# Kernel optimization log

Hardware: AMD Instinct MI355X
Metric: run time of the kernel (lower is better)

Reference implementation:

```python
import jax, jax.numpy as jnp
import numpy as np
from jax import lax

E, L, S, F = 4, 8, 512, 32
SAMPLE_SIZE = 512
BATCH_LEN = 64
TRAIN_ENVS = [0, 1, 2]


def setup_inputs() -> dict:
    key = jax.random.key(0)
    k1, k2 = jax.random.split(key)
    data_len = jax.random.randint(k2, (E, L), S // 2, S + 1).astype(jnp.int32)
    matrix = jax.random.normal(k1, (E, L, S, F), dtype=jnp.float32)
    # zero-pad samples beyond each (env,label) length, as shape_to_matrix does
    mask = (jnp.arange(S)[None, None, :, None] < data_len[:, :, None, None])
    matrix = matrix * mask.astype(jnp.float32)
    params = jnp.eye(F, dtype=jnp.float32)
    return {"matrix": matrix, "params": params, "data_len": data_len}


def _pair_indices():
    train_idx, test_idx = [], []
    for i in range(E):
        for j in range(E):
            idx = i * E + j
            if i < j:
                test_idx.append(idx)
                if i in TRAIN_ENVS and j in TRAIN_ENVS:
                    train_idx.append(idx)
    return np.array(train_idx), np.array(test_idx)


def reference(matrix, params, data_len):
    # normalize by mean per-(env,label,feature) std (torch.std is unbiased -> ddof=1)
    std = jnp.std(matrix, axis=2, ddof=1).mean()
    m = matrix / std
    bw = 1.06 * (S ** (-1.0 / 5.0)) * jnp.std(m, axis=2, ddof=1).mean()
    lenf = data_len.astype(jnp.float32)                     # [E,L]
    proj = jnp.einsum('elsf,fg->elsg', m, params)           # [E,L,S,F]

    left = lax.stop_gradient(proj.min())
    right = lax.stop_gradient(proj.max())
    delta = (right - left) / SAMPLE_SIZE
    grid = jnp.linspace(left, right, SAMPLE_SIZE)           # [G]
    divisor = jnp.sqrt(2.0 * jnp.pi) * bw

    n_chunks = SAMPLE_SIZE // BATCH_LEN
    grid_chunks = grid.reshape(n_chunks, BATCH_LEN)
    inv2bw2 = 0.5 / (bw * bw)
    pad_count = (float(S) - lenf)[:, :, None, None]         # [E,L,1,1]
    lend = lenf[:, :, None, None]

    def step(carry, pts):
        # Gaussian KDE kernel: offset^(d^2) == exp(-0.5*d^2/bw^2)
        d2 = (proj[..., None] - pts) ** 2                   # [E,L,S,F,C]
        ksum = jnp.exp(-inv2bw2 * d2).sum(axis=2)           # [E,L,F,C]
        corr = pad_count * jnp.exp(-inv2bw2 * pts ** 2)     # zero-padding correction
        red = (ksum - corr) / lend                          # [E,L,F,C]
        diff = jnp.abs(red[:, None] - red[None, :]).sum(-1) # [E,E,L,F]
        return carry + diff, None

    store, _ = lax.scan(step, jnp.zeros((E, E, L, F), dtype=proj.dtype), grid_chunks)
    store_dis = (store / divisor).reshape(E * E, L, F)

    train_idx, test_idx = _pair_indices()
    test_results = (store_dis[test_idx] * delta / 2.0).max(axis=0)    # [L,F]
    train_results = (store_dis[train_idx] * delta / 2.0).max(axis=0)  # [L,F]
    train_dis = train_results.max(axis=0).mean()
    test_dis = test_results.max(axis=0).mean()
    return train_results, test_results, train_dis, test_dis
```

## Files before the change

kernel.cpp:

```cpp
#include <hip/hip_runtime.h>
#include <float.h>


#if __has_builtin(__builtin_amdgcn_exp2f)
__device__ __forceinline__ float fast_exp2(float x) { return __builtin_amdgcn_exp2f(x); }
#else
__device__ __forceinline__ float fast_exp2(float x) { return exp2f(x); }
#endif

#define PT_OFF    0
#define SX_OFF    524288
#define SXX_OFF   532480
#define MIN_OFF   540672
#define MAX_OFF   540928
#define CNT_OFF   541184

__global__ __launch_bounds__(256) void stage_prep(const float* __restrict__ matrix,
                                                  const float* __restrict__ params,
                                                  float* __restrict__ PT,
                                                  float* __restrict__ sxg,
                                                  float* __restrict__ sxxg,
                                                  float* __restrict__ minp,
                                                  float* __restrict__ maxp,
                                                  int* __restrict__ counter) {
    __shared__ float M[64][33];
    __shared__ float Pm[32][32];
    __shared__ float sxr[8][32], sxxr[8][32];
    __shared__ float rmin[4], rmax[4];
    const int bid = blockIdx.x;
    const int s0 = (bid & 7) << 6;
    const int el = bid >> 3;
    const int t = threadIdx.x;
    if (bid == 0 && t == 0) *counter = 0;
    {
        const float4 v = reinterpret_cast<const float4*>(params)[t];
        const int base = t << 2;
        Pm[base >> 5][base & 31]       = v.x;
        Pm[base >> 5][(base & 31) + 1] = v.y;
        Pm[base >> 5][(base & 31) + 2] = v.z;
        Pm[base >> 5][(base & 31) + 3] = v.w;
    }
    const float4* mb4 = reinterpret_cast<const float4*>(matrix + (size_t)(el * 512 + s0) * 32);
    #pragma unroll
    for (int k = t; k < 512; k += 256) {
        const float4 v = mb4[k];
        const int base = k << 2;
        M[base >> 5][base & 31]       = v.x;
        M[base >> 5][(base & 31) + 1] = v.y;
        M[base >> 5][(base & 31) + 2] = v.z;
        M[base >> 5][(base & 31) + 3] = v.w;
    }
    __syncthreads();
    {
        const int f = t & 31, r = t >> 5;
        float sx = 0.f, sxx = 0.f;
        #pragma unroll
        for (int k = 0; k < 8; ++k) {
            float v = M[r * 8 + k][f];
            sx += v; sxx += v * v;
        }
        sxr[r][f] = sx; sxxr[r][f] = sxx;
    }
    const int s = t & 63;
    const int g0 = t >> 6;
    float lmin = FLT_MAX, lmax = -FLT_MAX;
    #pragma unroll
    for (int pass = 0; pass < 8; ++pass) {
        const int g = (pass << 2) + g0;
        float acc = 0.f;
        #pragma unroll
        for (int fp = 0; fp < 32; ++fp) acc += M[s][fp] * Pm[fp][g];
        lmin = fminf(lmin, acc);
        lmax = fmaxf(lmax, acc);
        PT[(size_t)(el * 32 + g) * 512 + s0 + s] = acc;
    }
    #pragma unroll
    for (int off = 32; off >= 1; off >>= 1) {
        lmin = fminf(lmin, __shfl_xor(lmin, off, 64));
        lmax = fmaxf(lmax, __shfl_xor(lmax, off, 64));
    }
    if ((t & 63) == 0) { rmin[t >> 6] = lmin; rmax[t >> 6] = lmax; }
    __syncthreads();
    if (t < 32) {
        float a = 0.f, b = 0.f;
        #pragma unroll
        for (int r = 0; r < 8; ++r) { a += sxr[r][t]; b += sxxr[r][t]; }
        sxg[bid * 32 + t] = a;
        sxxg[bid * 32 + t] = b;
    }
    if (t == 0) {
        minp[bid] = fminf(fminf(rmin[0], rmin[1]), fminf(rmin[2], rmin[3]));
        maxp[bid] = fmaxf(fmaxf(rmax[0], rmax[1]), fmaxf(rmax[2], rmax[3]));
    }
}

__global__ __launch_bounds__(512) void stage_kde2(const float* __restrict__ PT,
                                                  const float* __restrict__ sxg,
                                                  const float* __restrict__ sxxg,
                                                  const float* __restrict__ minp,
                                                  const float* __restrict__ maxp,
                                                  const int* __restrict__ dlen,
                                                  int* __restrict__ counter,
                                                  float* __restrict__ out) {
    __shared__ __align__(16) float xs[4][512];
    __shared__ float red[4][512];
    __shared__ float wsum[8], wmn[8], wmx[8];
    __shared__ float wred[8][6];
    __shared__ float csh[6];
    __shared__ int lastf;
    const int t = threadIdx.x;
    const int lf = blockIdx.x;
    const int l = lf >> 5, f = lf & 31;

    {
        float sf = 0.f;
        #pragma unroll
        for (int tr = t; tr < 1024; tr += 512) {
            const int el = tr >> 5, fc = tr & 31;
            const int base = el * 256 + fc;
            float Sx = 0.f, Sxx = 0.f;
            #pragma unroll
            for (int tile = 0; tile < 8; ++tile) { Sx += sxg[base + tile * 32]; Sxx += sxxg[base + tile * 32]; }
            const float mean = Sx * (1.0f / 512.0f);
            const float var = (Sxx - Sx * mean) * (1.0f / 511.0f);
            sf += sqrtf(fmaxf(var, 0.f));
        }
        float mn = (t < 256) ? minp[t] : FLT_MAX;
        float mx = (t < 256) ? maxp[t] : -FLT_MAX;
        #pragma unroll
        for (int off = 32; off >= 1; off >>= 1) {
            sf += __shfl_xor(sf, off, 64);
            mn = fminf(mn, __shfl_xor(mn, off, 64));
            mx = fmaxf(mx, __shfl_xor(mx, off, 64));
        }
        if ((t & 63) == 0) { wsum[t >> 6] = sf; wmn[t >> 6] = mn; wmx[t >> 6] = mx; }
        __syncthreads();
        if (t == 0) {
            float s = 0.f, lo = FLT_MAX, hi = -FLT_MAX;
            #pragma unroll
            for (int w = 0; w < 8; ++w) {
                s += wsum[w]; lo = fminf(lo, wmn[w]); hi = fmaxf(hi, wmx[w]);
            }
            const float stdv = s * (1.0f / 1024.0f);
            const float left  = lo / stdv;
            const float right = hi / stdv;
            const float bw = 1.06f * 0.28717458874925877f;
            const float delta = (right - left) * (1.0f / 512.0f);
            const float gstep = (right - left) * (1.0f / 511.0f);
            const float divisor = 2.5066282746310002f * bw;
            const float cpos = (0.5f / (bw * bw)) * 1.4426950408889634f;
            const float kf = sqrtf(cpos);
            csh[0] = left;
            csh[1] = gstep;
            csh[2] = kf;
            csh[3] = (1.0f / stdv) * kf;
            csh[4] = delta * 0.5f / divisor;
        }
    }
    __syncthreads();
    const float left = csh[0], gstep = csh[1], kf = csh[2], xscale = csh[3];

    #pragma unroll
    for (int k = t; k < 2048; k += 512) {
        const int e2 = k >> 9, s2 = k & 511;
        xs[e2][s2] = PT[((size_t)(((e2 << 3) + l) * 32 + f) << 9) + s2] * xscale;
    }
    __syncthreads();

    const int e = t >> 7, gl = t & 127;
    const int len = dlen[(e << 3) + l];
    float p[4];
    #pragma unroll
    for (int j = 0; j < 4; ++j)
        p[j] = fmaf((float)(gl + 128 * j), gstep, left) * kf;
    const float* __restrict__ x = xs[e];
    float acc[4][2];
    #pragma unroll
    for (int j = 0; j < 4; ++j) { acc[j][0] = 0.f; acc[j][1] = 0.f; }
    const int len4 = len & ~3;
    int s = 0;
    if (len4 > 0) {
        float4 v = *reinterpret_cast<const float4*>(&x[0]);
        for (s = 4; s < len4; s += 4) {
            const float4 nv = *reinterpret_cast<const float4*>(&x[s]);
            #pragma unroll
            for (int j = 0; j < 4; ++j) {
                const float d0 = v.x - p[j], d1 = v.y - p[j];
                const float d2 = v.z - p[j], d3 = v.w - p[j];
                acc[j][0] += fast_exp2(-(d0 * d0));
                acc[j][1] += fast_exp2(-(d1 * d1));
                acc[j][0] += fast_exp2(-(d2 * d2));
                acc[j][1] += fast_exp2(-(d3 * d3));
            }
            v = nv;
        }
        #pragma unroll
        for (int j = 0; j < 4; ++j) {
            const float d0 = v.x - p[j], d1 = v.y - p[j];
            const float d2 = v.z - p[j], d3 = v.w - p[j];
            acc[j][0] += fast_exp2(-(d0 * d0));
            acc[j][1] += fast_exp2(-(d1 * d1));
            acc[j][0] += fast_exp2(-(d2 * d2));
            acc[j][1] += fast_exp2(-(d3 * d3));
        }
        s = len4;
    }
    for (; s < len; ++s) {
        const float xv = x[s];
        #pragma unroll
        for (int j = 0; j < 4; ++j) {
            const float d = xv - p[j];
            acc[j][0] += fast_exp2(-(d * d));
        }
    }
    const float inv_len = 1.0f / (float)len;
    #pragma unroll
    for (int j = 0; j < 4; ++j)
        red[e][gl + 128 * j] = (acc[j][0] + acc[j][1]) * inv_len;
    __syncthreads();

    {
        const float r0 = red[0][t], r1 = red[1][t], r2 = red[2][t], r3 = red[3][t];
        float pr[6];
        pr[0] = fabsf(r0 - r1);
        pr[1] = fabsf(r0 - r2);
        pr[2] = fabsf(r0 - r3);
        pr[3] = fabsf(r1 - r2);
        pr[4] = fabsf(r1 - r3);
        pr[5] = fabsf(r2 - r3);
        #pragma unroll
        for (int pi = 0; pi < 6; ++pi) {
            float v = pr[pi];
            #pragma unroll
            for (int off = 32; off >= 1; off >>= 1) v += __shfl_xor(v, off, 64);
            if ((t & 63) == 0) wred[t >> 6][pi] = v;
        }
    }
    __syncthreads();
    if (t == 0) {
        const float scale = csh[4];
        float v[6];
        #pragma unroll
        for (int pi = 0; pi < 6; ++pi) {
            float sm = 0.f;
            #pragma unroll
            for (int w = 0; w < 8; ++w) sm += wred[w][pi];
            v[pi] = sm * scale;
        }
        float testv = v[0];
        #pragma unroll
        for (int pi = 1; pi < 6; ++pi) testv = fmaxf(testv, v[pi]);
        const float trainv = fmaxf(fmaxf(v[0], v[1]), v[3]);
        out[lf] = trainv;
        out[256 + lf] = testv;
        __threadfence();
        const int old = __hip_atomic_fetch_add(counter, 1, __ATOMIC_ACQ_REL,
                                               __HIP_MEMORY_SCOPE_AGENT);
        lastf = (old == 255);
    }
    __syncthreads();

    if (lastf && t < 64) {
        const int ff = t & 31;
        const int base = (t >= 32) ? 256 : 0;
        float m = -FLT_MAX;
        #pragma unroll
        for (int ll = 0; ll < 8; ++ll) {
            const float val = __hip_atomic_load(&out[base + ll * 32 + ff],
                                                __ATOMIC_RELAXED, __HIP_MEMORY_SCOPE_AGENT);
            m = fmaxf(m, val);
        }
        #pragma unroll
        for (int off = 16; off >= 1; off >>= 1) m += __shfl_xor(m, off, 32);
        if (ff == 0) out[512 + (base ? 1 : 0)] = m * (1.0f / 32.0f);
    }
}

extern "C" void kernel_launch(void* const* d_in, const int* in_sizes, int n_in,
                              void* d_out, int out_size, void* d_ws, size_t ws_size,
                              hipStream_t stream) {
    (void)in_sizes; (void)n_in; (void)out_size; (void)ws_size;
    const float* matrix = (const float*)d_in[0];
    const float* params = (const float*)d_in[1];
    const int*   dlen   = (const int*)d_in[2];
    float* out = (float*)d_out;
    float* ws  = (float*)d_ws;
    float* PT   = ws + PT_OFF;
    float* sxg  = ws + SX_OFF;
    float* sxxg = ws + SXX_OFF;
    float* minp = ws + MIN_OFF;
    float* maxp = ws + MAX_OFF;
    int*   cnt  = (int*)(ws + CNT_OFF);

    hipLaunchKernelGGL(stage_prep, dim3(256), dim3(256), 0, stream,
                       matrix, params, PT, sxg, sxxg, minp, maxp, cnt);
    hipLaunchKernelGGL(stage_kde2, dim3(256), dim3(512), 0, stream,
                       PT, sxg, sxxg, minp, maxp, dlen, cnt, out);
}
```

Before: 101.6 us.

## Bucket-sort samples per env and cull distant samples in KDE sum

Each block now counting-sorts the scaled projected samples into 64 value buckets in shared memory using atomics. Each wavefront then sums the Gaussian kernel only over buckets within a fixed radius of its grid-point range instead of over all samples. This avoids evaluating exp2 on samples whose contribution is negligible. In exchange it adds histogram, prefix-scan and scatter passes with extra barriers, and truncating the kernel at radius 4 in scaled units (exp2(-16)) introduces a small approximation error.

```diff
diff --git a/kernel.cpp b/kernel.cpp
--- a/kernel.cpp
+++ b/kernel.cpp
@@ -7,6 +7,8 @@
 #else
 __device__ __forceinline__ float fast_exp2(float x) { return exp2f(x); }
 #endif
+
+#define CULL_R 4.0f
 
 #define PT_OFF    0
 #define SX_OFF    524288
@@ -102,15 +104,20 @@
                                                   const int* __restrict__ dlen,
                                                   int* __restrict__ counter,
                                                   float* __restrict__ out) {
-    __shared__ __align__(16) float xs[4][512];
-    __shared__ float red[4][512];
+    __shared__ __align__(16) float bufA[4][512];
+    __shared__ __align__(16) float bufS[4][512];
+    __shared__ int hist[4][64];
+    __shared__ int startb[4][65];
+    __shared__ int lensh[4];
     __shared__ float wsum[8], wmn[8], wmx[8];
     __shared__ float wred[8][6];
-    __shared__ float csh[6];
+    __shared__ float csh[8];
     __shared__ int lastf;
     const int t = threadIdx.x;
     const int lf = blockIdx.x;
     const int l = lf >> 5, f = lf & 31;
+
+    if (t < 4) lensh[t] = dlen[(t << 3) + l];
 
     {
         float sf = 0.f;
@@ -150,77 +157,96 @@
             const float divisor = 2.5066282746310002f * bw;
             const float cpos = (0.5f / (bw * bw)) * 1.4426950408889634f;
             const float kf = sqrtf(cpos);
-            csh[0] = left;
-            csh[1] = gstep;
-            csh[2] = kf;
-            csh[3] = (1.0f / stdv) * kf;
-            csh[4] = delta * 0.5f / divisor;
-        }
-    }
-    __syncthreads();
-    const float left = csh[0], gstep = csh[1], kf = csh[2], xscale = csh[3];
+            const float leftk = left * kf, rightk = right * kf;
+            csh[0] = leftk;
+            csh[1] = gstep * kf;
+            csh[2] = (1.0f / stdv) * kf;
+            csh[3] = delta * 0.5f / divisor;
+            csh[4] = leftk - 1e-3f;
+            csh[5] = 64.0f / (rightk - leftk + 2e-3f);
+        }
+    }
+    __syncthreads();
+    const float leftk = csh[0], gstepk = csh[1], xscale = csh[2];
+    const float blo_ = csh[4], binv_ = csh[5];
 
     #pragma unroll
     for (int k = t; k < 2048; k += 512) {
         const int e2 = k >> 9, s2 = k & 511;
-        xs[e2][s2] = PT[((size_t)(((e2 << 3) + l) * 32 + f) << 9) + s2] * xscale;
-    }
-    __syncthreads();
-
-    const int e = t >> 7, gl = t & 127;
-    const int len = dlen[(e << 3) + l];
-    float p[4];
-    #pragma unroll
-    for (int j = 0; j < 4; ++j)
-        p[j] = fmaf((float)(gl + 128 * j), gstep, left) * kf;
-    const float* __restrict__ x = xs[e];
-    float acc[4][2];
-    #pragma unroll
-    for (int j = 0; j < 4; ++j) { acc[j][0] = 0.f; acc[j][1] = 0.f; }
-    const int len4 = len & ~3;
-    int s = 0;
-    if (len4 > 0) {
-        float4 v = *reinterpret_cast<const float4*>(&x[0]);
-        for (s = 4; s < len4; s += 4) {
-            const float4 nv = *reinterpret_cast<const float4*>(&x[s]);
-            #pragma unroll
-            for (int j = 0; j < 4; ++j) {
-                const float d0 = v.x - p[j], d1 = v.y - p[j];
-                const float d2 = v.z - p[j], d3 = v.w - p[j];
-                acc[j][0] += fast_exp2(-(d0 * d0));
-                acc[j][1] += fast_exp2(-(d1 * d1));
-                acc[j][0] += fast_exp2(-(d2 * d2));
-                acc[j][1] += fast_exp2(-(d3 * d3));
+        bufA[e2][s2] = PT[((size_t)(((e2 << 3) + l) * 32 + f) << 9) + s2] * xscale;
+    }
+    if (t < 256) hist[t >> 6][t & 63] = 0;
+    __syncthreads();
+
+    #pragma unroll
+    for (int k = t; k < 2048; k += 512) {
+        const int e2 = k >> 9, s2 = k & 511;
+        if (s2 < lensh[e2]) {
+            int b = (int)((bufA[e2][s2] - blo_) * binv_);
+            b = max(0, min(63, b));
+            atomicAdd(&hist[e2][b], 1);
+        }
+    }
+    __syncthreads();
+    if (t < 4) {
+        int acc = 0;
+        startb[t][0] = 0;
+        for (int b = 0; b < 64; ++b) { acc += hist[t][b]; startb[t][b + 1] = acc; }
+    }
+    __syncthreads();
+    if (t < 256) hist[t >> 6][t & 63] = startb[t >> 6][t & 63];
+    __syncthreads();
+    #pragma unroll
+    for (int k = t; k < 2048; k += 512) {
+        const int e2 = k >> 9, s2 = k & 511;
+        if (s2 < lensh[e2]) {
+            const float X = bufA[e2][s2];
+            int b = (int)((X - blo_) * binv_);
+            b = max(0, min(63, b));
+            const int pos = atomicAdd(&hist[e2][b], 1);
+            bufS[e2][pos] = X;
+        }
+    }
+    __syncthreads();
+
+    {
+        const int e = t >> 7, gl = t & 127;
+        const int len = lensh[e];
+        const float inv_len = 1.0f / (float)len;
+        const int glA = gl & 64;
+        const float* __restrict__ x = bufS[e];
+        #pragma unroll
+        for (int j = 0; j < 4; ++j) {
+            const int jg = gl + 128 * j;
+            const float P = fmaf((float)jg, gstepk, leftk);
+            const float Plo = fmaf((float)(glA + 128 * j), gstepk, leftk) - CULL_R;
+            const float Phi = fmaf((float)(glA + 63 + 128 * j), gstepk, leftk) + CULL_R;
+            int blo = (int)((Plo - blo_) * binv_); blo = max(0, min(63, blo));
+            int bhi = (int)((Phi - blo_) * binv_); bhi = max(0, min(63, bhi));
+            const int slo = startb[e][blo] & ~3;
+            const int shi = startb[e][bhi + 1];
+            float a0 = 0.f, a1 = 0.f, a2 = 0.f, a3 = 0.f;
+            int s = slo;
+            for (; s + 4 <= shi; s += 4) {
+                const float4 v = *reinterpret_cast<const float4*>(&x[s]);
+                const float d0 = v.x - P, d1 = v.y - P;
+                const float d2 = v.z - P, d3 = v.w - P;
+                a0 += fast_exp2(-(d0 * d0));
+                a1 += fast_exp2(-(d1 * d1));
+                a2 += fast_exp2(-(d2 * d2));
+                a3 += fast_exp2(-(d3 * d3));
             }
-            v = nv;
-        }
-        #pragma unroll
-        for (int j = 0; j < 4; ++j) {
-            const float d0 = v.x - p[j], d1 = v.y - p[j];
-            const float d2 = v.z - p[j], d3 = v.w - p[j];
-            acc[j][0] += fast_exp2(-(d0 * d0));
-            acc[j][1] += fast_exp2(-(d1 * d1));
-            acc[j][0] += fast_exp2(-(d2 * d2));
-            acc[j][1] += fast_exp2(-(d3 * d3));
-        }
-        s = len4;
-    }
-    for (; s < len; ++s) {
-        const float xv = x[s];
-        #pragma unroll
-        for (int j = 0; j < 4; ++j) {
-            const float d = xv - p[j];
-            acc[j][0] += fast_exp2(-(d * d));
-        }
-    }
-    const float inv_len = 1.0f / (float)len;
-    #pragma unroll
-    for (int j = 0; j < 4; ++j)
-        red[e][gl + 128 * j] = (acc[j][0] + acc[j][1]) * inv_len;
-    __syncthreads();
-
-    {
-        const float r0 = red[0][t], r1 = red[1][t], r2 = red[2][t], r3 = red[3][t];
+            for (; s < shi; ++s) {
+                const float d = x[s] - P;
+                a0 += fast_exp2(-(d * d));
+            }
+            bufA[e][jg] = ((a0 + a1) + (a2 + a3)) * inv_len;
+        }
+    }
+    __syncthreads();
+
+    {
+        const float r0 = bufA[0][t], r1 = bufA[1][t], r2 = bufA[2][t], r3 = bufA[3][t];
         float pr[6];
         pr[0] = fabsf(r0 - r1);
         pr[1] = fabsf(r0 - r2);
@@ -238,7 +264,7 @@
     }
     __syncthreads();
     if (t == 0) {
-        const float scale = csh[4];
+        const float scale = csh[3];
         float v[6];
         #pragma unroll
         for (int pi = 0; pi < 6; ++pi) {
```

New measurement: 93.91 us. -7.5%, faster.

## Replace direct KDE summation with linear binning and truncated Gaussian convolution

Applied to the files above, without the earlier changes.

Samples are linearly binned onto the evaluation grid using integer LDS atomics with fixed-point weights. Each grid point's density is then computed as a symmetric convolution with precomputed Gaussian weights truncated at about 3.5 bandwidths. This removes the per-sample-per-gridpoint exp evaluations that dominated the KDE stage. In exchange it introduces binning and truncation approximation error and adds LDS atomics and extra synchronisation.

```diff
diff --git a/kernel.cpp b/kernel.cpp
--- a/kernel.cpp
+++ b/kernel.cpp
@@ -7,6 +7,10 @@
 #else
 __device__ __forceinline__ float fast_exp2(float x) { return exp2f(x); }
 #endif
+
+#define MAXR 160
+#define PADL 160
+#define HW   840
 
 #define PT_OFF    0
 #define SX_OFF    524288
@@ -94,7 +98,7 @@
     }
 }
 
-__global__ __launch_bounds__(512) void stage_kde2(const float* __restrict__ PT,
+__global__ __launch_bounds__(512) void stage_kde3(const float* __restrict__ PT,
                                                   const float* __restrict__ sxg,
                                                   const float* __restrict__ sxxg,
                                                   const float* __restrict__ minp,
@@ -102,15 +106,25 @@
                                                   const int* __restrict__ dlen,
                                                   int* __restrict__ counter,
                                                   float* __restrict__ out) {
-    __shared__ __align__(16) float xs[4][512];
-    __shared__ float red[4][512];
+    __shared__ int   histI[4][HW];
+    __shared__ float fine[4][512];
+    __shared__ float wsh[MAXR + 4];
     __shared__ float wsum[8], wmn[8], wmx[8];
     __shared__ float wred[8][6];
-    __shared__ float csh[6];
-    __shared__ int lastf;
+    __shared__ float csh[8];
+    __shared__ int   Rsh;
+    __shared__ int   lensh[4];
+    __shared__ int   lastf;
     const int t = threadIdx.x;
     const int lf = blockIdx.x;
     const int l = lf >> 5, f = lf & 31;
+
+    if (t < 4) lensh[t] = dlen[(t << 3) + l];
+    {
+        int* hflat = &histI[0][0];
+        #pragma unroll
+        for (int k = t; k < 4 * HW; k += 512) hflat[k] = 0;
+    }
 
     {
         float sf = 0.f;
@@ -150,77 +164,84 @@
             const float divisor = 2.5066282746310002f * bw;
             const float cpos = (0.5f / (bw * bw)) * 1.4426950408889634f;
             const float kf = sqrtf(cpos);
-            csh[0] = left;
-            csh[1] = gstep;
-            csh[2] = kf;
-            csh[3] = (1.0f / stdv) * kf;
-            csh[4] = delta * 0.5f / divisor;
-        }
-    }
-    __syncthreads();
-    const float left = csh[0], gstep = csh[1], kf = csh[2], xscale = csh[3];
+            const float h = gstep * kf;
+            csh[0] = left * kf;
+            csh[1] = h;
+            csh[2] = (1.0f / stdv) * kf;
+            csh[3] = delta * 0.5f / divisor;
+            csh[5] = 1.0f / h;
+            Rsh = min((int)(3.5f / h) + 1, MAXR);
+        }
+    }
+    __syncthreads();
+    const float h = csh[1];
+    const int R = Rsh;
+
+    if (t <= R) {
+        const float u = (float)t * h;
+        wsh[t] = fast_exp2(-(u * u));
+    }
+
+    const int e = t >> 7;
+    {
+        const int sbase = (t & 127) << 2;
+        const int lenE = lensh[e];
+        const size_t row = ((size_t)(((e << 3) + l) * 32 + f) << 9);
+        const float4 xv = *reinterpret_cast<const float4*>(&PT[row + sbase]);
+        const float A = csh[2] * csh[5];
+        const float B = csh[0] * csh[5];
+        float uu[4] = { fmaf(xv.x, A, -B), fmaf(xv.y, A, -B),
+                        fmaf(xv.z, A, -B), fmaf(xv.w, A, -B) };
+        #pragma unroll
+        for (int q = 0; q < 4; ++q) {
+            if (sbase + q < lenE) {
+                const float u = fminf(fmaxf(uu[q], 0.f), 511.f);
+                const int   b = (int)u;
+                const float fr = u - (float)b;
+                const int w1 = (int)(fr * 16384.f + 0.5f);
+                atomicAdd(&histI[e][PADL + b], 16384 - w1);
+                atomicAdd(&histI[e][PADL + b + 1], w1);
+            }
+        }
+    }
+    __syncthreads();
 
     #pragma unroll
-    for (int k = t; k < 2048; k += 512) {
-        const int e2 = k >> 9, s2 = k & 511;
-        xs[e2][s2] = PT[((size_t)(((e2 << 3) + l) * 32 + f) << 9) + s2] * xscale;
-    }
-    __syncthreads();
-
-    const int e = t >> 7, gl = t & 127;
-    const int len = dlen[(e << 3) + l];
-    float p[4];
-    #pragma unroll
-    for (int j = 0; j < 4; ++j)
-        p[j] = fmaf((float)(gl + 128 * j), gstep, left) * kf;
-    const float* __restrict__ x = xs[e];
-    float acc[4][2];
-    #pragma unroll
-    for (int j = 0; j < 4; ++j) { acc[j][0] = 0.f; acc[j][1] = 0.f; }
-    const int len4 = len & ~3;
-    int s = 0;
-    if (len4 > 0) {
-        float4 v = *reinterpret_cast<const float4*>(&x[0]);
-        for (s = 4; s < len4; s += 4) {
-            const float4 nv = *reinterpret_cast<const float4*>(&x[s]);
-            #pragma unroll
-            for (int j = 0; j < 4; ++j) {
-                const float d0 = v.x - p[j], d1 = v.y - p[j];
-                const float d2 = v.z - p[j], d3 = v.w - p[j];
-                acc[j][0] += fast_exp2(-(d0 * d0));
-                acc[j][1] += fast_exp2(-(d1 * d1));
-                acc[j][0] += fast_exp2(-(d2 * d2));
-                acc[j][1] += fast_exp2(-(d3 * d3));
-            }
-            v = nv;
-        }
-        #pragma unroll
-        for (int j = 0; j < 4; ++j) {
-            const float d0 = v.x - p[j], d1 = v.y - p[j];
-            const float d2 = v.z - p[j], d3 = v.w - p[j];
-            acc[j][0] += fast_exp2(-(d0 * d0));
-            acc[j][1] += fast_exp2(-(d1 * d1));
-            acc[j][0] += fast_exp2(-(d2 * d2));
-            acc[j][1] += fast_exp2(-(d3 * d3));
-        }
-        s = len4;
-    }
-    for (; s < len; ++s) {
-        const float xv = x[s];
-        #pragma unroll
-        for (int j = 0; j < 4; ++j) {
-            const float d = xv - p[j];
-            acc[j][0] += fast_exp2(-(d * d));
-        }
-    }
-    const float inv_len = 1.0f / (float)len;
-    #pragma unroll
-    for (int j = 0; j < 4; ++j)
-        red[e][gl + 128 * j] = (acc[j][0] + acc[j][1]) * inv_len;
-    __syncthreads();
-
-    {
-        const float r0 = red[0][t], r1 = red[1][t], r2 = red[2][t], r3 = red[3][t];
+    for (int e2 = 0; e2 < 4; ++e2) {
+        const float ce = (1.0f / 16384.0f) / (float)lensh[e2];
+        for (int k = t; k < HW; k += 512) {
+            const int iv = histI[e2][k];
+            *reinterpret_cast<float*>(&histI[e2][k]) = (float)iv * ce;
+        }
+    }
+    __syncthreads();
+
+    {
+        const float* __restrict__ hf = reinterpret_cast<const float*>(&histI[e][0]);
+        const int g0 = t & 127;
+        const int c0 = PADL + g0;
+        const int c1 = c0 + 128;
+        const int c2 = c0 + 256;
+        const int c3 = c0 + 384;
+        const float w0 = wsh[0];
+        float a0 = w0 * hf[c0], a1 = w0 * hf[c1];
+        float a2 = w0 * hf[c2], a3 = w0 * hf[c3];
+        for (int d = 1; d <= R; ++d) {
+            const float wd = wsh[d];
+            a0 += wd * (hf[c0 + d] + hf[c0 - d]);
+            a1 += wd * (hf[c1 + d] + hf[c1 - d]);
+            a2 += wd * (hf[c2 + d] + hf[c2 - d]);
+            a3 += wd * (hf[c3 + d] + hf[c3 - d]);
+        }
+        fine[e][g0]       = a0;
+        fine[e][g0 + 128] = a1;
+        fine[e][g0 + 256] = a2;
+        fine[e][g0 + 384] = a3;
+    }
+    __syncthreads();
+
+    {
+        const float r0 = fine[0][t], r1 = fine[1][t], r2 = fine[2][t], r3 = fine[3][t];
         float pr[6];
         pr[0] = fabsf(r0 - r1);
         pr[1] = fabsf(r0 - r2);
@@ -238,7 +259,7 @@
     }
     __syncthreads();
     if (t == 0) {
-        const float scale = csh[4];
+        const float scale = csh[3];
         float v[6];
         #pragma unroll
         for (int pi = 0; pi < 6; ++pi) {
@@ -294,6 +315,6 @@
 
     hipLaunchKernelGGL(stage_prep, dim3(256), dim3(256), 0, stream,
                        matrix, params, PT, sxg, sxxg, minp, maxp, cnt);
-    hipLaunchKernelGGL(stage_kde2, dim3(256), dim3(512), 0, stream,
+    hipLaunchKernelGGL(stage_kde3, dim3(256), dim3(512), 0, stream,
                        PT, sxg, sxxg, minp, maxp, dlen, cnt, out);
 }
```

Result: faster. 83.77 us (-17.5%).
